# Performance work log

Measured on AMD Instinct MI355X. Metric: run time of the kernel, lower is better.

Reference implementation:

```python
import jax, jax.numpy as jnp
import numpy as np

# locally-connected conv constants (match init_kwargs)
SH, SW = 2, 2      # stride
KH, KW = 8, 8      # kernel dims
PH, PW = 0, 0      # padding


def setup_inputs() -> dict:
    key = jax.random.key(0)
    k1, k2 = jax.random.split(key)
    x = jax.random.normal(k1, (16, 3, 128, 128), dtype=jnp.float32)
    # untied weights: one [OC, C, KH, KW] filter per output location (61x61 grid)
    W = jax.random.normal(k2, (61, 61, 64, 3, 8, 8), dtype=jnp.float32) * 0.05
    bias = jnp.zeros((64, 61, 61), dtype=jnp.float32)
    return {"x": x, "W": W, "bias": bias}


def reference(x, W, bias):
    B = x.shape[0]
    NH, NW, OC = W.shape[0], W.shape[1], W.shape[2]
    xp = jnp.pad(x, ((0, 0), (0, 0), (PH, PH), (PW, PW)))
    # gather all patches at once: rows[NH,KH], cols[NW,KW]
    rows = (jnp.arange(NH) * SH)[:, None] + jnp.arange(KH)
    cols = (jnp.arange(NW) * SW)[:, None] + jnp.arange(KW)
    # patches: [B, C, NH, NW, KH, KW]
    patches = xp[:, :, rows[:, None, :, None], cols[None, :, None, :]]
    # per-location matmul (untied conv): out [B, OC, NH, NW]
    out = jnp.einsum('bchwij,hwocij->bohw', patches, W) + bias[None]
    # flatten_into_2D: interleave sqrt(OC) x sqrt(OC) channel blocks into spatial map
    r = int(np.sqrt(OC))  # 8
    o = out.transpose(0, 2, 3, 1).reshape(B, NH, NW, r, r)
    o = o.transpose(0, 1, 3, 2, 4).reshape(B, r * NH, r * NW)
    return o[:, None]  # [B, 1, r*NH, r*NW]
```

## Files before the change

kernel.cpp:

```cpp
#include <hip/hip_runtime.h>


namespace {
constexpr int NHW  = 61 * 61;
constexpr int XB   = 3 * 128 * 128;
constexpr int XCC  = 128 * 128;
constexpr int OSTR = 488 * 488;
}

typedef __fp16   fp16x2 __attribute__((ext_vector_type(2)));
typedef _Float16 half8v __attribute__((ext_vector_type(8)));
typedef float    f32x4  __attribute__((ext_vector_type(4)));

union H8 { fp16x2 p[4]; half8v h; uint4 u; };

__global__ __launch_bounds__(128, 4) void lc2d_kernel(
    const float* __restrict__ xg,
    const float* __restrict__ wg,
    const float* __restrict__ bg,
    float* __restrict__ og)
{
    __shared__ __align__(16) _Float16 wlh[32 * 192];
    __shared__ __align__(16) _Float16 xlh[16 * 192];

    const int bid  = blockIdx.x;
    const int hw   = bid >> 1;
    const int half = bid & 1;
    const int h    = hw / 61;
    const int w    = hw - h * 61;
    const int t    = threadIdx.x;
    const int lane = t & 63;
    const int wv   = t >> 6;

    {
        const float* wbase = wg + ((size_t)hw * 64 + half * 32) * 192;
        #pragma unroll
        for (int it = 0; it < 6; ++it) {
            const int g  = it * 128 + t;
            const int oc = g / 24;
            const int s8 = g - oc * 24;
            const float* src = wbase + oc * 192 + s8 * 8;
            const float4 va = *reinterpret_cast<const float4*>(src);
            const float4 vb = *reinterpret_cast<const float4*>(src + 4);
            H8 u;
            u.p[0] = __builtin_amdgcn_cvt_pkrtz(va.x, va.y);
            u.p[1] = __builtin_amdgcn_cvt_pkrtz(va.z, va.w);
            u.p[2] = __builtin_amdgcn_cvt_pkrtz(vb.x, vb.y);
            u.p[3] = __builtin_amdgcn_cvt_pkrtz(vb.z, vb.w);
            int srot = s8 + (oc & 7); if (srot >= 24) srot -= 24;
            *reinterpret_cast<uint4*>(&wlh[oc * 192 + srot * 8]) = u.u;
        }
    }
    {
        const float* xb = xg + (h * 2) * 128 + (w * 2);
        #pragma unroll
        for (int it = 0; it < 3; ++it) {
            const int g  = it * 128 + t;
            const int b  = g / 24;
            const int s8 = g - b * 24;
            const int c  = s8 >> 3;
            const int i  = s8 & 7;
            const float* src = xb + b * XB + c * XCC + i * 128;
            const float2 e0 = *reinterpret_cast<const float2*>(src);
            const float2 e1 = *reinterpret_cast<const float2*>(src + 2);
            const float2 e2 = *reinterpret_cast<const float2*>(src + 4);
            const float2 e3 = *reinterpret_cast<const float2*>(src + 6);
            H8 u;
            u.p[0] = __builtin_amdgcn_cvt_pkrtz(e0.x, e0.y);
            u.p[1] = __builtin_amdgcn_cvt_pkrtz(e1.x, e1.y);
            u.p[2] = __builtin_amdgcn_cvt_pkrtz(e2.x, e2.y);
            u.p[3] = __builtin_amdgcn_cvt_pkrtz(e3.x, e3.y);
            int srot = s8 + (b & 7); if (srot >= 24) srot -= 24;
            *reinterpret_cast<uint4*>(&xlh[b * 192 + srot * 8]) = u.u;
        }
    }
    __syncthreads();

    const int lq  = lane & 15;
    const int lk  = lane >> 4;
    const int ocl = wv * 16 + lq;

    f32x4 acc = {0.f, 0.f, 0.f, 0.f};
    #pragma unroll
    for (int ks = 0; ks < 6; ++ks) {
        const int slog = ks * 4 + lk;
        int sa = slog + (lq & 7);  if (sa >= 24) sa -= 24;
        int sb = slog + (ocl & 7); if (sb >= 24) sb -= 24;
        const half8v av = *reinterpret_cast<const half8v*>(&xlh[lq  * 192 + sa * 8]);
        const half8v bv = *reinterpret_cast<const half8v*>(&wlh[ocl * 192 + sb * 8]);
        acc = __builtin_amdgcn_mfma_f32_16x16x32_f16(av, bv, acc, 0, 0, 0);
    }

    const int   ocg = half * 32 + ocl;
    const float bz  = bg[ocg * NHW + hw];
    float* ob = og + (h * 8 + (ocg >> 3)) * 488 + (w * 8 + (ocg & 7));
    #pragma unroll
    for (int r = 0; r < 4; ++r) {
        const int b = lk * 4 + r;
        ob[(size_t)b * OSTR] = acc[r] + bz;
    }
}

extern "C" void kernel_launch(void* const* d_in, const int* in_sizes, int n_in,
                              void* d_out, int out_size, void* d_ws, size_t ws_size,
                              hipStream_t stream) {
    const float* x    = (const float*)d_in[0];
    const float* W    = (const float*)d_in[1];
    const float* bias = (const float*)d_in[2];
    float* out        = (float*)d_out;
    lc2d_kernel<<<dim3(NHW * 2), dim3(128), 0, stream>>>(x, W, bias, out);
}
```

Before: 44.22 us.

## Merge OC halves into one 256-thread block and batch all global loads first

Each block now handles all 64 output channels of one output location with 256 threads, instead of two 128-thread blocks each doing 32 channels. This halves the redundant input-patch loads and the block count. All weight and input global loads are issued into registers before any conversion or LDS store, with a sched_barrier between the two phases, so more memory requests are in flight at once. The input patch is now loaded as float2 chunks spread across more threads. The cost is higher register pressure from the 12 float4 and 6 float2 staging values, and double the LDS per block.

```diff
diff --git a/kernel.cpp b/kernel.cpp
--- a/kernel.cpp
+++ b/kernel.cpp
@@ -14,65 +14,73 @@
 
 union H8 { fp16x2 p[4]; half8v h; uint4 u; };
 
-__global__ __launch_bounds__(128, 4) void lc2d_kernel(
+__global__ __launch_bounds__(256, 5) void lc2d_kernel(
     const float* __restrict__ xg,
     const float* __restrict__ wg,
     const float* __restrict__ bg,
     float* __restrict__ og)
 {
-    __shared__ __align__(16) _Float16 wlh[32 * 192];
+    __shared__ __align__(16) _Float16 wlh[64 * 192];
     __shared__ __align__(16) _Float16 xlh[16 * 192];
 
-    const int bid  = blockIdx.x;
-    const int hw   = bid >> 1;
-    const int half = bid & 1;
+    const int hw   = blockIdx.x;
     const int h    = hw / 61;
     const int w    = hw - h * 61;
     const int t    = threadIdx.x;
     const int lane = t & 63;
     const int wv   = t >> 6;
 
-    {
-        const float* wbase = wg + ((size_t)hw * 64 + half * 32) * 192;
-        #pragma unroll
-        for (int it = 0; it < 6; ++it) {
-            const int g  = it * 128 + t;
-            const int oc = g / 24;
-            const int s8 = g - oc * 24;
-            const float* src = wbase + oc * 192 + s8 * 8;
-            const float4 va = *reinterpret_cast<const float4*>(src);
-            const float4 vb = *reinterpret_cast<const float4*>(src + 4);
-            H8 u;
-            u.p[0] = __builtin_amdgcn_cvt_pkrtz(va.x, va.y);
-            u.p[1] = __builtin_amdgcn_cvt_pkrtz(va.z, va.w);
-            u.p[2] = __builtin_amdgcn_cvt_pkrtz(vb.x, vb.y);
-            u.p[3] = __builtin_amdgcn_cvt_pkrtz(vb.z, vb.w);
-            int srot = s8 + (oc & 7); if (srot >= 24) srot -= 24;
-            *reinterpret_cast<uint4*>(&wlh[oc * 192 + srot * 8]) = u.u;
-        }
+    const float* wbase = wg + (size_t)hw * (64 * 192);
+    const float* xb    = xg + (h * 2) * 128 + (w * 2);
+
+    float4 wr[12];
+    #pragma unroll
+    for (int it = 0; it < 6; ++it) {
+        const int g  = it * 256 + t;
+        const int oc = g / 24;
+        const int s8 = g - oc * 24;
+        const float* src = wbase + oc * 192 + s8 * 8;
+        wr[it * 2]     = *reinterpret_cast<const float4*>(src);
+        wr[it * 2 + 1] = *reinterpret_cast<const float4*>(src + 4);
     }
-    {
-        const float* xb = xg + (h * 2) * 128 + (w * 2);
-        #pragma unroll
-        for (int it = 0; it < 3; ++it) {
-            const int g  = it * 128 + t;
-            const int b  = g / 24;
-            const int s8 = g - b * 24;
-            const int c  = s8 >> 3;
-            const int i  = s8 & 7;
-            const float* src = xb + b * XB + c * XCC + i * 128;
-            const float2 e0 = *reinterpret_cast<const float2*>(src);
-            const float2 e1 = *reinterpret_cast<const float2*>(src + 2);
-            const float2 e2 = *reinterpret_cast<const float2*>(src + 4);
-            const float2 e3 = *reinterpret_cast<const float2*>(src + 6);
-            H8 u;
-            u.p[0] = __builtin_amdgcn_cvt_pkrtz(e0.x, e0.y);
-            u.p[1] = __builtin_amdgcn_cvt_pkrtz(e1.x, e1.y);
-            u.p[2] = __builtin_amdgcn_cvt_pkrtz(e2.x, e2.y);
-            u.p[3] = __builtin_amdgcn_cvt_pkrtz(e3.x, e3.y);
-            int srot = s8 + (b & 7); if (srot >= 24) srot -= 24;
-            *reinterpret_cast<uint4*>(&xlh[b * 192 + srot * 8]) = u.u;
-        }
+    float2 xr[6];
+    #pragma unroll
+    for (int it = 0; it < 6; ++it) {
+        const int f  = it * 256 + t;
+        const int b  = f / 96;
+        const int r  = f - b * 96;
+        const int k  = r * 2;
+        const int c  = k >> 6;
+        const int i  = (k >> 3) & 7;
+        const int j  = k & 7;
+        xr[it] = *reinterpret_cast<const float2*>(xb + b * XB + c * XCC + i * 128 + j);
+    }
+    __builtin_amdgcn_sched_barrier(0);
+
+    #pragma unroll
+    for (int it = 0; it < 6; ++it) {
+        const int g  = it * 256 + t;
+        const int oc = g / 24;
+        const int s8 = g - oc * 24;
+        H8 u;
+        u.p[0] = __builtin_amdgcn_cvt_pkrtz(wr[it*2].x,   wr[it*2].y);
+        u.p[1] = __builtin_amdgcn_cvt_pkrtz(wr[it*2].z,   wr[it*2].w);
+        u.p[2] = __builtin_amdgcn_cvt_pkrtz(wr[it*2+1].x, wr[it*2+1].y);
+        u.p[3] = __builtin_amdgcn_cvt_pkrtz(wr[it*2+1].z, wr[it*2+1].w);
+        int srot = s8 + (oc & 7); if (srot >= 24) srot -= 24;
+        *reinterpret_cast<uint4*>(&wlh[oc * 192 + srot * 8]) = u.u;
+    }
+    #pragma unroll
+    for (int it = 0; it < 6; ++it) {
+        const int f  = it * 256 + t;
+        const int b  = f / 96;
+        const int r  = f - b * 96;
+        const int s8 = r >> 2;
+        const int j  = (r & 3) * 2;
+        const fp16x2 pk = __builtin_amdgcn_cvt_pkrtz(xr[it].x, xr[it].y);
+        int srot = s8 + (b & 7); if (srot >= 24) srot -= 24;
+        union { fp16x2 p; unsigned u; } cv; cv.p = pk;
+        *reinterpret_cast<unsigned*>(&xlh[b * 192 + srot * 8 + j]) = cv.u;
     }
     __syncthreads();
 
@@ -84,16 +92,15 @@
     #pragma unroll
     for (int ks = 0; ks < 6; ++ks) {
         const int slog = ks * 4 + lk;
-        int sa = slog + (lq & 7);  if (sa >= 24) sa -= 24;
-        int sb = slog + (ocl & 7); if (sb >= 24) sb -= 24;
+        int sa = slog + (lq & 7);   if (sa >= 24) sa -= 24;
+        int sb = slog + (ocl & 7);  if (sb >= 24) sb -= 24;
         const half8v av = *reinterpret_cast<const half8v*>(&xlh[lq  * 192 + sa * 8]);
         const half8v bv = *reinterpret_cast<const half8v*>(&wlh[ocl * 192 + sb * 8]);
         acc = __builtin_amdgcn_mfma_f32_16x16x32_f16(av, bv, acc, 0, 0, 0);
     }
 
-    const int   ocg = half * 32 + ocl;
-    const float bz  = bg[ocg * NHW + hw];
-    float* ob = og + (h * 8 + (ocg >> 3)) * 488 + (w * 8 + (ocg & 7));
+    const float bz = bg[ocl * NHW + hw];
+    float* ob = og + (h * 8 + (ocl >> 3)) * 488 + (w * 8 + (ocl & 7));
     #pragma unroll
     for (int r = 0; r < 4; ++r) {
         const int b = lk * 4 + r;
@@ -108,5 +115,5 @@
     const float* W    = (const float*)d_in[1];
     const float* bias = (const float*)d_in[2];
     float* out        = (float*)d_out;
-    lc2d_kernel<<<dim3(NHW * 2), dim3(128), 0, stream>>>(x, W, bias, out);
+    lc2d_kernel<<<dim3(NHW), dim3(256), 0, stream>>>(x, W, bias, out);
 }
```

After: 39.66 us. -10.3%, faster.
